# Performance work log

Measured on AMD Instinct MI355X. Metric: run time of the kernel, lower is better.

## Reference

```python
import jax, jax.numpy as jnp
import numpy as np

PS = 32
NUM_ANG_BINS = 36

def _circular_gauss_kernel(kernlen):
    # Faithful to affnet Utils.CircularGaussKernel (sigma=None, norm=True)
    half = kernlen / 2.0
    r2 = half * half
    sigma2 = 0.9 * r2
    yy, xx = np.meshgrid(np.arange(kernlen), np.arange(kernlen), indexing='ij')
    disq = (yy - half) ** 2 + (xx - half) ** 2
    k = np.exp(-disq / sigma2)
    k = k / k.sum()
    return k.astype(np.float32)

def setup_inputs() -> dict:
    key = jax.random.key(0)
    B = 65536
    x = jax.random.uniform(key, (B, 1, PS, PS), dtype=jnp.float32)
    gk = jnp.asarray(10.0 * _circular_gauss_kernel(PS))  # [PS, PS]
    return {"x": x, "gk": gk}

def reference(x, gk):
    B = x.shape[0]
    nb = NUM_ANG_BINS
    # gx: conv with [0.5, 0, -0.5] on replicate-padded width
    xp = jnp.pad(x, ((0, 0), (0, 0), (0, 0), (1, 1)), mode='edge')
    gx = 0.5 * (xp[..., :-2] - xp[..., 2:])
    # gy: conv with [0.5, 0, -0.5]^T on replicate-padded height
    yp = jnp.pad(x, ((0, 0), (0, 0), (1, 1), (0, 0)), mode='edge')
    gy = 0.5 * (yp[..., :-2, :] - yp[..., 2:, :])
    mag = jnp.sqrt(gx * gx + gy * gy + 1e-10) * gk  # gk broadcasts over [B,1,PS,PS]
    ori = jnp.arctan2(gy, gx)
    o_big = nb * (ori + jnp.pi) / (2.0 * jnp.pi)
    bo0 = jnp.floor(o_big)
    wo1 = o_big - bo0
    bo0 = jnp.mod(bo0, nb).astype(jnp.int32)
    wo0 = (1.0 - wo1) * mag  # note: original forward only accumulates wo0 into bin bo0
    hw = PS * PS
    wo0f = wo0.reshape(B, hw)
    bo0f = bo0.reshape(B, hw)
    # single-pass scatter-add histogram, then mean (adaptive_avg_pool2d -> /HW)
    bins = jnp.zeros((B, nb), x.dtype).at[jnp.arange(B)[:, None], bo0f].add(wo0f) / hw
    # conv1d kernel [0.33, 0.34, 0.33], zero padding=1
    bp = jnp.pad(bins, ((0, 0), (1, 1)))
    sm = 0.33 * bp[:, :-2] + 0.34 * bp[:, 1:-1] + 0.33 * bp[:, 2:]
    idx = jnp.argmax(sm, axis=1)
    angle = -(2.0 * jnp.pi * idx.astype(x.dtype) / nb - jnp.pi)
    return angle
```

## Files before the change

### kernel.cpp

```cpp
#include <hip/hip_runtime.h>
#include <math.h>

#define NB 36

__device__ __forceinline__ double atan_ref64(double u) {
  bool hi = u > 0.41421356237309503;
  double q = hi ? (u - 1.0) / (u + 1.0) : u;
  double t = q * q;
  double R =      1.62858201153657823623e-02;
  R = fma(R, t, -3.65315727442169155270e-02);
  R = fma(R, t,  4.97687799461593236017e-02);
  R = fma(R, t, -5.83357013379057348645e-02);
  R = fma(R, t,  6.66107313738753120669e-02);
  R = fma(R, t, -7.69187620504482999495e-02);
  R = fma(R, t,  9.09088713343650656196e-02);
  R = fma(R, t, -1.11111104054623557880e-01);
  R = fma(R, t,  1.42857142725034663711e-01);
  R = fma(R, t, -1.99999999998764832476e-01);
  R = fma(R, t,  3.33333333333329318027e-01);
  double h = t * R;
  double a = fma(-h, q, q);
  return hi ? (0.7853981633974483 + a) : a;
}

__device__ __forceinline__ float atan2f_fast(float gyf, float gxf,
                                             const double* __restrict__ atab) {
  float axf = fabsf(gxf);
  float ayf = fabsf(gyf);
  float mnf = fminf(axf, ayf);
  float mxf = fmaxf(axf, ayf);
  float mxg = (mxf == 0.0f) ? 1.0f : mxf;
  const bool swp = ayf > axf;

  float r0 = __builtin_amdgcn_rcpf(mxg);
  float c8 = rintf(mnf * (8.0f * r0));
  int   k  = (int)c8;
  float cf = c8 * 0.125f;

  double mn = (double)mnf, mx = (double)mxg, cd = (double)cf;
  double num = fma(-cd, mx, mn);
  double den = fma( cd, mn, mx);

  float denf = fmaf(cf, mnf, mxg);
  double rd = (double)__builtin_amdgcn_rcpf(denf);
  rd = fma(fma(-den, rd, 1.0), rd, rd);
  double q = num * rd;
  double t = q * q;

  float tf = (float)t;
  float V = fmaf(-tf, fmaf(-tf, 1.0f/11.0f, 1.0f/9.0f), 1.0f/7.0f);
  double S = fma(-t, (double)V, 0.2);
  double R = fma(-t, S, 1.0/3.0);
  double h = t * R;
  double a = fma(-h, q, q);

  a = atab[k] + a;
  a = swp         ? (1.5707963267948966 - a) : a;
  a = (gxf < 0.0f)? (3.141592653589793  - a) : a;
  return copysignf((float)a, gyf);
}

#define PX(L, R, UP, DN, G) do {                                    \
    float gx_ = 0.5f * ((L) - (R));                                 \
    float gy_ = 0.5f * ((UP) - (DN));                               \
    float m2_ = fmaf(gy_, gy_, fmaf(gx_, gx_, 1e-10f));             \
    float mag_ = __builtin_amdgcn_sqrtf(m2_) * (G);                 \
    float ori_ = atan2f_fast(gy_, gx_, atab);                       \
    float s1_ = ori_ + PI_F;                                        \
    float d2_ = 36.0f * s1_;                                        \
    float q0_ = d2_ * C_INV_TPI;       \
    float rm_ = fmaf(-TPI_F, q0_, d2_);                             \
    float ob_ = fmaf(rm_, C_INV_TPI, q0_);                          \
    float fo_ = floorf(ob_);                                        \
    float wo1_ = ob_ - fo_;                                         \
    int b0_ = (int)fo_;                                             \
    if (b0_ >= NB) b0_ -= NB;                                       \
    h[b0_] += fmaf(-wo1_, mag_, mag_);                              \
  } while (0)

#define QUAD(cq, uq, dq, gq, LV, RV) do {                           \
    PX(LV,   cq.y, uq.x, dq.x, gq.x);                               \
    PX(cq.x, cq.z, uq.y, dq.y, gq.y);                               \
    PX(cq.y, cq.w, uq.z, dq.z, gq.z);                               \
    PX(cq.z, RV,   uq.w, dq.w, gq.w);                               \
  } while (0)

#define UP1(v) __shfl_up((v), 1, 32)
#define DN1(v) __shfl_down((v), 1, 32)

__global__ __launch_bounds__(256, 4) void orient_kernel(
    const float* __restrict__ x,
    const float* __restrict__ gk,
    float* __restrict__ out)
{
#pragma clang fp contract(off)
  __shared__ float hist[256 * 37];
  __shared__ double atab[9];

  const int t    = threadIdx.x;
  const int lane = t & 63;
  const int row  = lane & 31;
  const int half = lane >> 5;
  const int p    = (blockIdx.x * 256 + t) >> 6;

  const float PI_F  = 3.14159265358979323846f;
  const float TPI_F = 6.28318530717958647692f;
  const float C_INV_TPI = (float)(1.0 / (double)6.28318530717958647692f);

  if (t < 9) atab[t] = atan_ref64((double)t * 0.125);

  float* __restrict__ h = &hist[t * 37];
  #pragma unroll
  for (int b = 0; b < NB; ++b) h[b] = 0.0f;

  __syncthreads();

  const float4* __restrict__ xv =
      (const float4*)(x + (size_t)p * 1024 + (row * 32 + half * 16));
  const float4* __restrict__ gv = (const float4*)(gk + (row * 32 + half * 16));
  float4 c0 = xv[0], c1 = xv[1], c2 = xv[2], c3 = xv[3];
  float4 g0 = gv[0], g1 = gv[1], g2 = gv[2], g3 = gv[3];

  float4 u0, u1, u2, u3, d0, d1, d2, d3;
  u0.x=UP1(c0.x); u0.y=UP1(c0.y); u0.z=UP1(c0.z); u0.w=UP1(c0.w);
  u1.x=UP1(c1.x); u1.y=UP1(c1.y); u1.z=UP1(c1.z); u1.w=UP1(c1.w);
  u2.x=UP1(c2.x); u2.y=UP1(c2.y); u2.z=UP1(c2.z); u2.w=UP1(c2.w);
  u3.x=UP1(c3.x); u3.y=UP1(c3.y); u3.z=UP1(c3.z); u3.w=UP1(c3.w);
  d0.x=DN1(c0.x); d0.y=DN1(c0.y); d0.z=DN1(c0.z); d0.w=DN1(c0.w);
  d1.x=DN1(c1.x); d1.y=DN1(c1.y); d1.z=DN1(c1.z); d1.w=DN1(c1.w);
  d2.x=DN1(c2.x); d2.y=DN1(c2.y); d2.z=DN1(c2.z); d2.w=DN1(c2.w);
  d3.x=DN1(c3.x); d3.y=DN1(c3.y); d3.z=DN1(c3.z); d3.w=DN1(c3.w);

  float send = half ? c0.x : c3.w;
  float recv = __shfl_xor(send, 32, 64);
  float LB = half ? recv : c0.x;
  float RB = half ? c3.w : recv;

  QUAD(c0, u0, d0, g0, LB,   c1.x);
  QUAD(c1, u1, d1, g1, c0.w, c2.x);
  QUAD(c2, u2, d2, g2, c1.w, c3.x);
  QUAD(c3, u3, d3, g3, c2.w, RB);

  __builtin_amdgcn_wave_barrier();

  const float* __restrict__ hw = &hist[(t >> 6) * 2368];
  const int bb = (lane < NB) ? lane : NB - 1;
  float s = 0.0f;
  #pragma unroll
  for (int k = 0; k < 64; ++k) {
    const int l = (k >> 1) + ((k & 1) << 5);
    s += hw[l * 37 + bb];
  }

  float ll = __shfl(s, lane - 1);
  float rr = __shfl(s, lane + 1);
  float v; int idx;
  if (lane < NB) {
    float sl = (lane > 0)      ? ll : 0.0f;
    float sr = (lane < NB - 1) ? rr : 0.0f;
    v = (0.33f * sl + 0.34f * s) + 0.33f * sr;
    idx = lane;
  } else {
    v = -INFINITY; idx = 1 << 20;
  }
  #pragma unroll
  for (int off = 32; off > 0; off >>= 1) {
    float v2 = __shfl_xor(v, off, 64);
    int   i2 = __shfl_xor(idx, off, 64);
    if (v2 > v || (v2 == v && i2 < idx)) { v = v2; idx = i2; }
  }
  if (lane == 0) {
    out[p] = -((TPI_F * (float)idx) / 36.0f - PI_F);
  }
}

extern "C" void kernel_launch(void* const* d_in, const int* in_sizes, int n_in,
                              void* d_out, int out_size, void* d_ws, size_t ws_size,
                              hipStream_t stream) {
  const float* x  = (const float*)d_in[0];
  const float* gk = (const float*)d_in[1];
  float* out = (float*)d_out;
  const int B = in_sizes[0] / 1024;
  orient_kernel<<<B / 4, 256, 0, stream>>>(x, gk, out);
}
```

Measured before the change: 399.6 us.

## Replace FP64 atan2 with float double-float arithmetic and 512-entry quadrant table

The FP64 reduction and polynomial in atan2 are replaced by double-float (hi/lo float pair) arithmetic. A finer 128-step table that already folds in the quadrant offsets is built by a separate init kernel and copied into shared memory per block. The per-thread histogram stride also changes from 37 to 36 floats. The aim is to drop the FP64 instructions, at the cost of an extra launch, a larger shared-memory table, possible bank conflicts from the 36-float stride, and a risk of bin-boundary precision mismatches against the reference.

```diff
diff --git a/kernel.cpp b/kernel.cpp
--- a/kernel.cpp
+++ b/kernel.cpp
@@ -23,41 +23,68 @@
   return hi ? (0.7853981633974483 + a) : a;
 }
 
-__device__ __forceinline__ float atan2f_fast(float gyf, float gxf,
-                                             const double* __restrict__ atab) {
+__device__ float2 g_atab[512];
+
+__global__ void init_atab(void) {
+  int t = threadIdx.x;
+  int j = t >> 7, k = t & 127;
+  double th = atan_ref64((double)k * 0.0078125);
+  double C = (j == 0) ? 0.0 : (j == 2) ? 3.141592653589793 : 1.5707963267948966;
+  double s = (j == 0 || j == 3) ? 1.0 : -1.0;
+  double v = C + s * th;
+  float hi = (float)v;
+  float lo = (float)(v - (double)hi);
+  g_atab[t] = make_float2(hi, lo);
+}
+
+__device__ __forceinline__ float atan2f_dd(float gyf, float gxf,
+                                           const float2* __restrict__ atab) {
   float axf = fabsf(gxf);
   float ayf = fabsf(gyf);
   float mnf = fminf(axf, ayf);
   float mxf = fmaxf(axf, ayf);
   float mxg = (mxf == 0.0f) ? 1.0f : mxf;
-  const bool swp = ayf > axf;
+  const bool swp   = ayf > axf;
+  const bool gxneg = gxf < 0.0f;
+  const int  j     = (swp ? 1 : 0) | (gxneg ? 2 : 0);
+  const int  smask = (swp != gxneg) ? 0x80000000 : 0;
 
   float r0 = __builtin_amdgcn_rcpf(mxg);
-  float c8 = rintf(mnf * (8.0f * r0));
-  int   k  = (int)c8;
-  float cf = c8 * 0.125f;
-
-  double mn = (double)mnf, mx = (double)mxg, cd = (double)cf;
-  double num = fma(-cd, mx, mn);
-  double den = fma( cd, mn, mx);
-
-  float denf = fmaf(cf, mnf, mxg);
-  double rd = (double)__builtin_amdgcn_rcpf(denf);
-  rd = fma(fma(-den, rd, 1.0), rd, rd);
-  double q = num * rd;
-  double t = q * q;
-
-  float tf = (float)t;
-  float V = fmaf(-tf, fmaf(-tf, 1.0f/11.0f, 1.0f/9.0f), 1.0f/7.0f);
-  double S = fma(-t, (double)V, 0.2);
-  double R = fma(-t, S, 1.0/3.0);
-  double h = t * R;
-  double a = fma(-h, q, q);
-
-  a = atab[k] + a;
-  a = swp         ? (1.5707963267948966 - a) : a;
-  a = (gxf < 0.0f)? (3.141592653589793  - a) : a;
-  return copysignf((float)a, gyf);
+  float cm = fminf(rintf((mnf * r0) * 128.0f), 127.0f);
+  int   k  = (int)cm;
+  float cf = cm * 0.0078125f;
+
+  float ph = cf * mxg;
+  float pl = fmaf(cf, mxg, -ph);
+  float nh = mnf - ph;
+  nh = __int_as_float(__float_as_int(nh) ^ smask);
+  pl = __int_as_float(__float_as_int(pl) ^ smask);
+
+  float ph2 = cf * mnf;
+  float pl2 = fmaf(cf, mnf, -ph2);
+  float dh  = mxg + ph2;
+  float dl  = ((mxg - dh) + ph2) + pl2;
+
+  float rA  = __builtin_amdgcn_rcpf(dh);
+  float e   = fmaf(-dh, rA, 1.0f);
+  float em  = fmaf(-dl, rA, e);
+  float qh  = nh * rA;
+  float plo = fmaf(nh, rA, -qh);
+  float ql  = fmaf(qh, em, plo);
+  ql = fmaf(-pl, rA, ql);
+
+  float qs = qh + ql;
+  float t  = qs * qs;
+  float S  = fmaf(-t, 0.14285715f, 0.2f);
+  float Rp = fmaf(-t, S, 0.33333334f);
+  float cu = qs * (t * Rp);
+
+  float2 T = atab[(j << 7) | k];
+  float hh = T.x + qh;
+  float e1 = (T.x - hh) + qh;
+  float lo = ((ql - cu) + T.y) + e1;
+  float f  = hh + lo;
+  return copysignf(f, gyf);
 }
 
 #define PX(L, R, UP, DN, G) do {                                    \
@@ -65,7 +92,7 @@
     float gy_ = 0.5f * ((UP) - (DN));                               \
     float m2_ = fmaf(gy_, gy_, fmaf(gx_, gx_, 1e-10f));             \
     float mag_ = __builtin_amdgcn_sqrtf(m2_) * (G);                 \
-    float ori_ = atan2f_fast(gy_, gx_, atab);                       \
+    float ori_ = atan2f_dd(gy_, gx_, atabl);                        \
     float s1_ = ori_ + PI_F;                                        \
     float d2_ = 36.0f * s1_;                                        \
     float q0_ = d2_ * C_INV_TPI;       \
@@ -94,8 +121,8 @@
     float* __restrict__ out)
 {
 #pragma clang fp contract(off)
-  __shared__ float hist[256 * 37];
-  __shared__ double atab[9];
+  __shared__ float  hist[256 * 36];
+  __shared__ float2 atabl[512];
 
   const int t    = threadIdx.x;
   const int lane = t & 63;
@@ -107,9 +134,10 @@
   const float TPI_F = 6.28318530717958647692f;
   const float C_INV_TPI = (float)(1.0 / (double)6.28318530717958647692f);
 
-  if (t < 9) atab[t] = atan_ref64((double)t * 0.125);
-
-  float* __restrict__ h = &hist[t * 37];
+  atabl[t]       = g_atab[t];
+  atabl[t + 256] = g_atab[t + 256];
+
+  float* __restrict__ h = &hist[t * 36];
   #pragma unroll
   for (int b = 0; b < NB; ++b) h[b] = 0.0f;
 
@@ -143,13 +171,13 @@
 
   __builtin_amdgcn_wave_barrier();
 
-  const float* __restrict__ hw = &hist[(t >> 6) * 2368];
+  const float* __restrict__ hw = &hist[(t >> 6) * 2304];
   const int bb = (lane < NB) ? lane : NB - 1;
   float s = 0.0f;
   #pragma unroll
   for (int k = 0; k < 64; ++k) {
     const int l = (k >> 1) + ((k & 1) << 5);
-    s += hw[l * 37 + bb];
+    s += hw[l * 36 + bb];
   }
 
   float ll = __shfl(s, lane - 1);
@@ -181,5 +209,6 @@
   const float* gk = (const float*)d_in[1];
   float* out = (float*)d_out;
   const int B = in_sizes[0] / 1024;
+  init_atab<<<1, 512, 0, stream>>>();
   orient_kernel<<<B / 4, 256, 0, stream>>>(x, gk, out);
 }
```

Result: no change. 400.0 us (+0.1%).
